# Kernel tuning notes

Measured on AMD Instinct MI355X. Metric: run time of the kernel, lower is better.

## Reference

```python
import jax, jax.numpy as jnp
import numpy as np

EPS = 1e-5


def _segment_norm(x, seg, num_segments):
    # x: [N, D], seg: [N] sorted segment ids in [0, num_segments)
    ones = jnp.ones((x.shape[0],), x.dtype)
    cnt = jax.ops.segment_sum(ones, seg, num_segments=num_segments)      # [B]
    safe = jnp.maximum(cnt, 1.0)[:, None]                                # avoid 0-div
    mean = jax.ops.segment_sum(x, seg, num_segments=num_segments) / safe # [B, D]
    centered = x - mean[seg]
    var = jax.ops.segment_sum(centered * centered, seg, num_segments=num_segments) / safe
    std = jnp.sqrt(var)                                                  # unbiased=False
    normed = centered / (std[seg] + EPS)
    # graphs with a single element are passed through unchanged
    return jnp.where((cnt > 1.0)[seg][:, None], normed, x)


def setup_inputs() -> dict:
    key = jax.random.key(0)
    k1, k2, k3, k4 = jax.random.split(key, 4)
    N, D, B = 1_000_000, 128, 1024
    node_feat = jax.random.normal(k1, (N, D), dtype=jnp.float32)
    edge_feat = jax.random.normal(k2, (N, D), dtype=jnp.float32)
    node_seg = jnp.sort(jax.random.randint(k3, (N,), 0, B, dtype=jnp.int32))
    edge_seg = jnp.sort(jax.random.randint(k4, (N,), 0, B, dtype=jnp.int32))
    return {
        "node_feat": node_feat,
        "edge_feat": edge_feat,
        "node_gamma": jnp.ones((D,), jnp.float32),
        "node_beta": jnp.zeros((D,), jnp.float32),
        "edge_gamma": jnp.ones((D,), jnp.float32),
        "edge_beta": jnp.zeros((D,), jnp.float32),
        "node_seg": node_seg,
        "edge_seg": edge_seg,
        "num_graphs": B,
    }


def reference(node_feat, edge_feat, node_gamma, node_beta, edge_gamma, edge_beta,
              node_seg, edge_seg, num_graphs):
    node_out = _segment_norm(node_feat, node_seg, num_graphs) * node_gamma + node_beta
    edge_out = _segment_norm(edge_feat, edge_seg, num_graphs) * edge_gamma + edge_beta
    return (node_out, edge_out)
```

## Files before the change

### kernel.cpp

```cpp
#include <hip/hip_runtime.h>


static constexpr int   D4     = 32;
static constexpr int   CHUNK  = 64;
static constexpr int   NCHUNK = 4;
static constexpr int   TILE_W = CHUNK * NCHUNK;
static constexpr int   TILE_B = TILE_W * 4;
static constexpr int   DEPTH  = 3;
static constexpr float EPS    = 1e-5f;

typedef float vfloat4 __attribute__((ext_vector_type(4)));

#define WAITV(N) do { asm volatile("s_waitcnt vmcnt(" #N ")" ::: "memory"); \
                      __builtin_amdgcn_sched_barrier(0); } while (0)

__device__ __forceinline__ void waitv_dyn(int n) {
    switch (n) {
        case 0:  WAITV(0);  break;
        case 4:  WAITV(4);  break;
        case 8:  WAITV(8);  break;
        case 12: WAITV(12); break;
        default: WAITV(16); break;
    }
}

__device__ __forceinline__ void nt_store4(float4* p, const float4& v) {
    vfloat4 w = { v.x, v.y, v.z, v.w };
    __builtin_nontemporal_store(w, reinterpret_cast<vfloat4*>(p));
}

__device__ __forceinline__ void acc4(float4& s, float4& q, const float4& v) {
    s.x += v.x; s.y += v.y; s.z += v.z; s.w += v.w;
    q.x += v.x * v.x; q.y += v.y * v.y;
    q.z += v.z * v.z; q.w += v.w * v.w;
}

__device__ __forceinline__ float4 affine4(const float4& v, const float4& A,
                                          const float4& Bc) {
    float4 o;
    o.x = v.x * A.x + Bc.x; o.y = v.y * A.y + Bc.y;
    o.z = v.z * A.z + Bc.z; o.w = v.w * A.w + Bc.w;
    return o;
}

__global__ __launch_bounds__(256) void seg_norm_r11(
    const float4* __restrict__ xn, const float4* __restrict__ xe,
    const float*  __restrict__ gn, const float*  __restrict__ bn,
    const float*  __restrict__ ge, const float*  __restrict__ be,
    const int*    __restrict__ sn, const int*    __restrict__ se,
    float4* __restrict__ on, float4* __restrict__ oe,
    int N)
{
    __shared__ float4 ring[4][DEPTH][TILE_W];
    __shared__ float4 pS[4][32], pQ[4][32];
    __shared__ int    s_bounds[2];

    const bool is_edge = (blockIdx.y != 0);
    const float4* __restrict__ x   = is_edge ? xe : xn;
    const float*  __restrict__ gam = is_edge ? ge : gn;
    const float*  __restrict__ bet = is_edge ? be : bn;
    const int*    __restrict__ seg = is_edge ? se : sn;
    float4*       __restrict__ out = is_edge ? oe : on;

    const int b   = (int)blockIdx.x;
    const int tid = (int)threadIdx.x;

    if (tid < 2) {
        const int target = b + tid;
        int lo = 0, hi = N;
        while (lo < hi) {
            int mid = (lo + hi) >> 1;
            if (seg[mid] < target) lo = mid + 1; else hi = mid;
        }
        s_bounds[tid] = lo;
    }
    __syncthreads();
    const int start = s_bounds[0];
    const int end   = s_bounds[1];
    const int cnt   = end - start;
    if (cnt <= 0) return;

    const int w    = tid >> 6;
    const int lane = tid & 63;
    const int dg   = lane & 31;

    const size_t f4base = (size_t)start * D4;
    const int    f4cnt  = cnt * D4;
    const int    nt     = f4cnt / TILE_B;

    auto issue = [&](int t, float4* lp) {
        const float4* gp = x + f4base + (size_t)t * TILE_B + w * TILE_W + lane;
        #pragma unroll
        for (int i = 0; i < NCHUNK; ++i)
            __builtin_amdgcn_global_load_lds(gp + i * CHUNK, lp + i * CHUNK, 16, 0, 0);
    };

    float4 s = make_float4(0.f, 0.f, 0.f, 0.f);
    float4 q = make_float4(0.f, 0.f, 0.f, 0.f);
    if (nt > 0) {
        const int pre = min(nt, DEPTH);
        for (int p = 0; p < pre; ++p) issue(p, &ring[w][p][0]);
        for (int t = 0; t < nt; ++t) {
            waitv_dyn(4 * min(DEPTH - 1, nt - 1 - t));
            float4* cur = &ring[w][t % DEPTH][0];
            #pragma unroll
            for (int i = 0; i < NCHUNK; ++i)
                acc4(s, q, cur[i * CHUNK + lane]);
            if (t + DEPTH < nt) issue(t + DEPTH, cur);
        }
    }
    for (int j = nt * TILE_B + tid; j < f4cnt; j += 256)
        acc4(s, q, x[f4base + j]);

    s.x += __shfl_down(s.x, 32); s.y += __shfl_down(s.y, 32);
    s.z += __shfl_down(s.z, 32); s.w += __shfl_down(s.w, 32);
    q.x += __shfl_down(q.x, 32); q.y += __shfl_down(q.y, 32);
    q.z += __shfl_down(q.z, 32); q.w += __shfl_down(q.w, 32);
    if (lane < 32) { pS[w][lane] = s; pQ[w][lane] = q; }
    __syncthreads();
    if (tid < 32) {
        float4 S = pS[0][tid], Q = pQ[0][tid];
        #pragma unroll
        for (int k = 1; k < 4; ++k) {
            const float4 a = pS[k][tid], c = pQ[k][tid];
            S.x += a.x; S.y += a.y; S.z += a.z; S.w += a.w;
            Q.x += c.x; Q.y += c.y; Q.z += c.z; Q.w += c.w;
        }
        const float rc = 1.0f / (float)cnt;
        float4 m, iv;
        m.x = S.x * rc; m.y = S.y * rc; m.z = S.z * rc; m.w = S.w * rc;
        iv.x = 1.0f / (sqrtf(fmaxf(Q.x * rc - m.x * m.x, 0.f)) + EPS);
        iv.y = 1.0f / (sqrtf(fmaxf(Q.y * rc - m.y * m.y, 0.f)) + EPS);
        iv.z = 1.0f / (sqrtf(fmaxf(Q.z * rc - m.z * m.z, 0.f)) + EPS);
        iv.w = 1.0f / (sqrtf(fmaxf(Q.w * rc - m.w * m.w, 0.f)) + EPS);
        if (cnt <= 1) {
            m  = make_float4(0.f, 0.f, 0.f, 0.f);
            iv = make_float4(1.f, 1.f, 1.f, 1.f);
        }
        const float4 g4 = ((const float4*)gam)[tid];
        const float4 b4 = ((const float4*)bet)[tid];
        float4 A, Bc;
        A.x = iv.x * g4.x; A.y = iv.y * g4.y; A.z = iv.z * g4.z; A.w = iv.w * g4.w;
        Bc.x = b4.x - m.x * A.x; Bc.y = b4.y - m.y * A.y;
        Bc.z = b4.z - m.z * A.z; Bc.w = b4.w - m.w * A.w;
        pS[0][tid] = A; pQ[0][tid] = Bc;
    }
    __syncthreads();
    const float4 A  = pS[0][dg];
    const float4 Bc = pQ[0][dg];

    if (nt > 0) {
        const int pre = min(nt, DEPTH);
        for (int p = 0; p < pre; ++p) issue(p, &ring[w][p][0]);
        for (int t = 0; t < nt; ++t) {
            waitv_dyn(4 * min(DEPTH - 1, nt - 1 - t) + 4 * min(DEPTH - 1, t));
            float4* cur = &ring[w][t % DEPTH][0];
            float4* op  = out + f4base + (size_t)t * TILE_B + w * TILE_W + lane;
            #pragma unroll
            for (int i = 0; i < NCHUNK; ++i)
                nt_store4(op + i * CHUNK, affine4(cur[i * CHUNK + lane], A, Bc));
            if (t + DEPTH < nt) issue(t + DEPTH, cur);
        }
    }
    for (int j = nt * TILE_B + tid; j < f4cnt; j += 256)
        nt_store4(&out[f4base + j], affine4(x[f4base + j], A, Bc));
}

extern "C" void kernel_launch(void* const* d_in, const int* in_sizes, int n_in,
                              void* d_out, int out_size, void* d_ws, size_t ws_size,
                              hipStream_t stream) {
    const float* node_feat  = (const float*)d_in[0];
    const float* edge_feat  = (const float*)d_in[1];
    const float* node_gamma = (const float*)d_in[2];
    const float* node_beta  = (const float*)d_in[3];
    const float* edge_gamma = (const float*)d_in[4];
    const float* edge_beta  = (const float*)d_in[5];
    const int*   node_seg   = (const int*)d_in[6];
    const int*   edge_seg   = (const int*)d_in[7];

    const int D = in_sizes[2];
    const int N = in_sizes[0] / D;
    const int B = 1024;

    float* out_node = (float*)d_out;
    float* out_edge = out_node + (size_t)N * (size_t)D;

    dim3 grid((unsigned)B, 2);
    seg_norm_r11<<<grid, 256, 0, stream>>>(
        (const float4*)node_feat, (const float4*)edge_feat,
        node_gamma, node_beta, edge_gamma, edge_beta,
        node_seg, edge_seg,
        (float4*)out_node, (float4*)out_edge, N);
}
```

Baseline: 566.5 us.

## Defer node-segment writeback to partner blocks via workspace flags and lagged scheduling

```diff
diff --git a/kernel.cpp b/kernel.cpp
--- a/kernel.cpp
+++ b/kernel.cpp
@@ -6,7 +6,7 @@
 static constexpr int   NCHUNK = 4;
 static constexpr int   TILE_W = CHUNK * NCHUNK;
 static constexpr int   TILE_B = TILE_W * 4;
-static constexpr int   DEPTH  = 3;
+static constexpr int   DEPTH  = 4;
 static constexpr float EPS    = 1e-5f;
 
 typedef float vfloat4 __attribute__((ext_vector_type(4)));
@@ -19,8 +19,7 @@
         case 0:  WAITV(0);  break;
         case 4:  WAITV(4);  break;
         case 8:  WAITV(8);  break;
-        case 12: WAITV(12); break;
-        default: WAITV(16); break;
+        default: WAITV(12); break;
     }
 }
 
@@ -43,47 +42,124 @@
     return o;
 }
 
-__global__ __launch_bounds__(256) void seg_norm_r11(
+__global__ __launch_bounds__(256) void seg_norm_lag(
     const float4* __restrict__ xn, const float4* __restrict__ xe,
     const float*  __restrict__ gn, const float*  __restrict__ bn,
     const float*  __restrict__ ge, const float*  __restrict__ be,
     const int*    __restrict__ sn, const int*    __restrict__ se,
     float4* __restrict__ on, float4* __restrict__ oe,
-    int N)
+    int* __restrict__ wsF, float4* __restrict__ wsA, float4* __restrict__ wsB,
+    int N, int lagmode)
 {
     __shared__ float4 ring[4][DEPTH][TILE_W];
     __shared__ float4 pS[4][32], pQ[4][32];
-    __shared__ int    s_bounds[2];
-
-    const bool is_edge = (blockIdx.y != 0);
-    const float4* __restrict__ x   = is_edge ? xe : xn;
-    const float*  __restrict__ gam = is_edge ? ge : gn;
-    const float*  __restrict__ bet = is_edge ? be : bn;
-    const int*    __restrict__ seg = is_edge ? se : sn;
-    float4*       __restrict__ out = is_edge ? oe : on;
-
-    const int b   = (int)blockIdx.x;
-    const int tid = (int)threadIdx.x;
-
-    if (tid < 2) {
-        const int target = b + tid;
-        int lo = 0, hi = N;
-        while (lo < hi) {
-            int mid = (lo + hi) >> 1;
-            if (seg[mid] < target) lo = mid + 1; else hi = mid;
-        }
-        s_bounds[tid] = lo;
-    }
-    __syncthreads();
-    const int start = s_bounds[0];
-    const int end   = s_bounds[1];
+    __shared__ float4 sAb[32], sBb[32];
+    __shared__ int    sm[4];
+
+    const int  bid  = (int)blockIdx.x;
+    const int  tid  = (int)threadIdx.x;
+    const int  w    = tid >> 6;
+    const int  lane = tid & 63;
+    const int  dg   = tid & 31;
+    const bool is_edge = (bid & 1);
+    const bool even    = !is_edge;
+
+    const float4* __restrict__ x    = is_edge ? xe : xn;
+    float4*       __restrict__ outp = is_edge ? oe : on;
+    const float*  __restrict__ gam  = is_edge ? ge : gn;
+    const float*  __restrict__ bet  = is_edge ? be : bn;
+    const int*    __restrict__ segp = is_edge ? se : sn;
+
+    auto bsearch2 = [&](const int* sg, int seg_id) {
+        if (tid < 2) {
+            const int target = seg_id + tid;
+            int lo = 0, hi = N;
+            while (lo < hi) {
+                int mid = (lo + hi) >> 1;
+                if (sg[mid] < target) lo = mid + 1; else hi = mid;
+            }
+            sm[tid] = lo;
+        }
+        __syncthreads();
+    };
+
+    auto fold_broadcast = [&](float4 s, float4 q, int cnt) {
+        s.x += __shfl_down(s.x, 32); s.y += __shfl_down(s.y, 32);
+        s.z += __shfl_down(s.z, 32); s.w += __shfl_down(s.w, 32);
+        q.x += __shfl_down(q.x, 32); q.y += __shfl_down(q.y, 32);
+        q.z += __shfl_down(q.z, 32); q.w += __shfl_down(q.w, 32);
+        if (lane < 32) { pS[w][lane] = s; pQ[w][lane] = q; }
+        __syncthreads();
+        if (tid < 32) {
+            float4 S = pS[0][tid], Q = pQ[0][tid];
+            #pragma unroll
+            for (int k = 1; k < 4; ++k) {
+                const float4 a = pS[k][tid], c = pQ[k][tid];
+                S.x += a.x; S.y += a.y; S.z += a.z; S.w += a.w;
+                Q.x += c.x; Q.y += c.y; Q.z += c.z; Q.w += c.w;
+            }
+            const float rc = 1.0f / (float)max(cnt, 1);
+            float4 m, iv;
+            m.x = S.x * rc; m.y = S.y * rc; m.z = S.z * rc; m.w = S.w * rc;
+            iv.x = 1.0f / (sqrtf(fmaxf(Q.x * rc - m.x * m.x, 0.f)) + EPS);
+            iv.y = 1.0f / (sqrtf(fmaxf(Q.y * rc - m.y * m.y, 0.f)) + EPS);
+            iv.z = 1.0f / (sqrtf(fmaxf(Q.z * rc - m.z * m.z, 0.f)) + EPS);
+            iv.w = 1.0f / (sqrtf(fmaxf(Q.w * rc - m.w * m.w, 0.f)) + EPS);
+            if (cnt <= 1) {
+                m  = make_float4(0.f, 0.f, 0.f, 0.f);
+                iv = make_float4(1.f, 1.f, 1.f, 1.f);
+            }
+            const float4 g4 = ((const float4*)gam)[tid];
+            const float4 b4 = ((const float4*)bet)[tid];
+            float4 A, Bc;
+            A.x = iv.x * g4.x; A.y = iv.y * g4.y;
+            A.z = iv.z * g4.z; A.w = iv.w * g4.w;
+            Bc.x = b4.x - m.x * A.x; Bc.y = b4.y - m.y * A.y;
+            Bc.z = b4.z - m.z * A.z; Bc.w = b4.w - m.w * A.w;
+            sAb[tid] = A; sBb[tid] = Bc;
+        }
+        __syncthreads();
+    };
+
+    auto bwrite = [&](const float4* src, float4* dst, size_t fb, int fc,
+                      float4 A, float4 Bc) {
+        int j = tid;
+        for (; j + 768 < fc; j += 1024) {
+            const float4 v0 = src[fb + j];
+            const float4 v1 = src[fb + j + 256];
+            const float4 v2 = src[fb + j + 512];
+            const float4 v3 = src[fb + j + 768];
+            nt_store4(&dst[fb + j],       affine4(v0, A, Bc));
+            nt_store4(&dst[fb + j + 256], affine4(v1, A, Bc));
+            nt_store4(&dst[fb + j + 512], affine4(v2, A, Bc));
+            nt_store4(&dst[fb + j + 768], affine4(v3, A, Bc));
+        }
+        for (; j < fc; j += 256)
+            nt_store4(&dst[fb + j], affine4(src[fb + j], A, Bc));
+    };
+
+    const bool has_partner = lagmode && even && (bid >= 512);
+    const int  pslot = (bid - 512) >> 1;
+    bool pre = false;
+    if (has_partner) {
+        if (tid == 0)
+            sm[2] = __hip_atomic_load(&wsF[pslot], __ATOMIC_ACQUIRE,
+                                      __HIP_MEMORY_SCOPE_AGENT);
+        __syncthreads();
+        pre = (sm[2] != 0);
+        if (pre) {
+            bsearch2(sn, pslot);
+            const int pst = sm[0], pen = sm[1];
+            const float4 A  = wsA[(size_t)pslot * 32 + dg];
+            const float4 Bc = wsB[(size_t)pslot * 32 + dg];
+            bwrite(xn, on, (size_t)pst * D4, (pen - pst) * D4, A, Bc);
+        }
+        __syncthreads();
+    }
+
+    bsearch2(segp, bid >> 1);
+    const int start = sm[0], end = sm[1];
     const int cnt   = end - start;
-    if (cnt <= 0) return;
-
-    const int w    = tid >> 6;
-    const int lane = tid & 63;
-    const int dg   = lane & 31;
-
     const size_t f4base = (size_t)start * D4;
     const int    f4cnt  = cnt * D4;
     const int    nt     = f4cnt / TILE_B;
@@ -98,11 +174,11 @@
     float4 s = make_float4(0.f, 0.f, 0.f, 0.f);
     float4 q = make_float4(0.f, 0.f, 0.f, 0.f);
     if (nt > 0) {
-        const int pre = min(nt, DEPTH);
-        for (int p = 0; p < pre; ++p) issue(p, &ring[w][p][0]);
+        const int preN = min(nt, DEPTH);
+        for (int p = 0; p < preN; ++p) issue(p, &ring[w][p][0]);
         for (int t = 0; t < nt; ++t) {
             waitv_dyn(4 * min(DEPTH - 1, nt - 1 - t));
-            float4* cur = &ring[w][t % DEPTH][0];
+            float4* cur = &ring[w][t & (DEPTH - 1)][0];
             #pragma unroll
             for (int i = 0; i < NCHUNK; ++i)
                 acc4(s, q, cur[i * CHUNK + lane]);
@@ -112,58 +188,60 @@
     for (int j = nt * TILE_B + tid; j < f4cnt; j += 256)
         acc4(s, q, x[f4base + j]);
 
-    s.x += __shfl_down(s.x, 32); s.y += __shfl_down(s.y, 32);
-    s.z += __shfl_down(s.z, 32); s.w += __shfl_down(s.w, 32);
-    q.x += __shfl_down(q.x, 32); q.y += __shfl_down(q.y, 32);
-    q.z += __shfl_down(q.z, 32); q.w += __shfl_down(q.w, 32);
-    if (lane < 32) { pS[w][lane] = s; pQ[w][lane] = q; }
-    __syncthreads();
-    if (tid < 32) {
-        float4 S = pS[0][tid], Q = pQ[0][tid];
-        #pragma unroll
-        for (int k = 1; k < 4; ++k) {
-            const float4 a = pS[k][tid], c = pQ[k][tid];
-            S.x += a.x; S.y += a.y; S.z += a.z; S.w += a.w;
-            Q.x += c.x; Q.y += c.y; Q.z += c.z; Q.w += c.w;
-        }
-        const float rc = 1.0f / (float)cnt;
-        float4 m, iv;
-        m.x = S.x * rc; m.y = S.y * rc; m.z = S.z * rc; m.w = S.w * rc;
-        iv.x = 1.0f / (sqrtf(fmaxf(Q.x * rc - m.x * m.x, 0.f)) + EPS);
-        iv.y = 1.0f / (sqrtf(fmaxf(Q.y * rc - m.y * m.y, 0.f)) + EPS);
-        iv.z = 1.0f / (sqrtf(fmaxf(Q.z * rc - m.z * m.z, 0.f)) + EPS);
-        iv.w = 1.0f / (sqrtf(fmaxf(Q.w * rc - m.w * m.w, 0.f)) + EPS);
-        if (cnt <= 1) {
-            m  = make_float4(0.f, 0.f, 0.f, 0.f);
-            iv = make_float4(1.f, 1.f, 1.f, 1.f);
-        }
-        const float4 g4 = ((const float4*)gam)[tid];
-        const float4 b4 = ((const float4*)bet)[tid];
+    fold_broadcast(s, q, cnt);
+
+    if (lagmode && even) {
+        const int slot = bid >> 1;
+        if (tid < 32) {
+            wsA[(size_t)slot * 32 + tid] = sAb[tid];
+            wsB[(size_t)slot * 32 + tid] = sBb[tid];
+        }
+        __threadfence();
+        if (tid == 0)
+            __hip_atomic_store(&wsF[slot], 1, __ATOMIC_RELEASE,
+                               __HIP_MEMORY_SCOPE_AGENT);
+    }
+
+    if (!lagmode || !even) {
+        bwrite(x, outp, f4base, f4cnt, sAb[dg], sBb[dg]);
+        return;
+    }
+
+    if (bid >= 1536)
+        bwrite(x, outp, f4base, f4cnt, sAb[dg], sBb[dg]);
+
+    if (has_partner && !pre) {
+        if (tid == 0) {
+            int got = 0;
+            for (int it = 0; it < 1200 && !got; ++it) {
+                got = __hip_atomic_load(&wsF[pslot], __ATOMIC_ACQUIRE,
+                                        __HIP_MEMORY_SCOPE_AGENT);
+                if (!got) __builtin_amdgcn_s_sleep(16);
+            }
+            sm[2] = got;
+        }
+        __syncthreads();
+        const bool got = (sm[2] != 0);
+        __syncthreads();
+        bsearch2(sn, pslot);
+        const int pst = sm[0], pen = sm[1];
+        const int pcnt = pen - pst;
+        const size_t pfb = (size_t)pst * D4;
+        const int    pfc = pcnt * D4;
         float4 A, Bc;
-        A.x = iv.x * g4.x; A.y = iv.y * g4.y; A.z = iv.z * g4.z; A.w = iv.w * g4.w;
-        Bc.x = b4.x - m.x * A.x; Bc.y = b4.y - m.y * A.y;
-        Bc.z = b4.z - m.z * A.z; Bc.w = b4.w - m.w * A.w;
-        pS[0][tid] = A; pQ[0][tid] = Bc;
-    }
-    __syncthreads();
-    const float4 A  = pS[0][dg];
-    const float4 Bc = pQ[0][dg];
-
-    if (nt > 0) {
-        const int pre = min(nt, DEPTH);
-        for (int p = 0; p < pre; ++p) issue(p, &ring[w][p][0]);
-        for (int t = 0; t < nt; ++t) {
-            waitv_dyn(4 * min(DEPTH - 1, nt - 1 - t) + 4 * min(DEPTH - 1, t));
-            float4* cur = &ring[w][t % DEPTH][0];
-            float4* op  = out + f4base + (size_t)t * TILE_B + w * TILE_W + lane;
-            #pragma unroll
-            for (int i = 0; i < NCHUNK; ++i)
-                nt_store4(op + i * CHUNK, affine4(cur[i * CHUNK + lane], A, Bc));
-            if (t + DEPTH < nt) issue(t + DEPTH, cur);
-        }
-    }
-    for (int j = nt * TILE_B + tid; j < f4cnt; j += 256)
-        nt_store4(&out[f4base + j], affine4(x[f4base + j], A, Bc));
+        if (got) {
+            A  = wsA[(size_t)pslot * 32 + dg];
+            Bc = wsB[(size_t)pslot * 32 + dg];
+        } else {
+            float4 fs = make_float4(0.f, 0.f, 0.f, 0.f);
+            float4 fq = make_float4(0.f, 0.f, 0.f, 0.f);
+            for (int j = tid; j < pfc; j += 256)
+                acc4(fs, fq, xn[pfb + j]);
+            fold_broadcast(fs, fq, pcnt);
+            A = sAb[dg]; Bc = sBb[dg];
+        }
+        bwrite(xn, on, pfb, pfc, A, Bc);
+    }
 }
 
 extern "C" void kernel_launch(void* const* d_in, const int* in_sizes, int n_in,
@@ -185,10 +263,18 @@
     float* out_node = (float*)d_out;
     float* out_edge = out_node + (size_t)N * (size_t)D;
 
-    dim3 grid((unsigned)B, 2);
-    seg_norm_r11<<<grid, 256, 0, stream>>>(
+    const size_t need = 4096 + 2ull * 1024 * 32 * sizeof(float4);
+    int lagmode = (ws_size >= need) ? 1 : 0;
+    int*    wsF = (int*)d_ws;
+    float4* wsA = (float4*)((char*)d_ws + 4096);
+    float4* wsB = wsA + 1024 * 32;
+    if (lagmode)
+        hipMemsetAsync(d_ws, 0, 4096, stream);
+
+    seg_norm_lag<<<dim3(2u * B), 256, 0, stream>>>(
         (const float4*)node_feat, (const float4*)edge_feat,
         node_gamma, node_beta, edge_gamma, edge_beta,
         node_seg, edge_seg,
-        (float4*)out_node, (float4*)out_edge, N);
-}
+        (float4*)out_node, (float4*)out_edge,
+        wsF, wsA, wsB, N, lagmode);
+}
```

New measurement: 965.7 us. 1.7x slower.

## Split segments across blocks, cache tile in registers, combine stats via atomics

Applied to the files above, without the earlier changes.

```diff
diff --git a/kernel.cpp b/kernel.cpp
--- a/kernel.cpp
+++ b/kernel.cpp
@@ -1,28 +1,12 @@
 #include <hip/hip_runtime.h>
 
 
-static constexpr int   D4     = 32;
-static constexpr int   CHUNK  = 64;
-static constexpr int   NCHUNK = 4;
-static constexpr int   TILE_W = CHUNK * NCHUNK;
-static constexpr int   TILE_B = TILE_W * 4;
-static constexpr int   DEPTH  = 3;
-static constexpr float EPS    = 1e-5f;
+static constexpr int   RV       = 32;
+static constexpr int   CHUNK_F4 = RV * 256;
+static constexpr int   CPS      = 5;
+static constexpr float EPS      = 1e-5f;
 
 typedef float vfloat4 __attribute__((ext_vector_type(4)));
-
-#define WAITV(N) do { asm volatile("s_waitcnt vmcnt(" #N ")" ::: "memory"); \
-                      __builtin_amdgcn_sched_barrier(0); } while (0)
-
-__device__ __forceinline__ void waitv_dyn(int n) {
-    switch (n) {
-        case 0:  WAITV(0);  break;
-        case 4:  WAITV(4);  break;
-        case 8:  WAITV(8);  break;
-        case 12: WAITV(12); break;
-        default: WAITV(16); break;
-    }
-}
 
 __device__ __forceinline__ void nt_store4(float4* p, const float4& v) {
     vfloat4 w = { v.x, v.y, v.z, v.w };
@@ -43,74 +27,71 @@
     return o;
 }
 
-__global__ __launch_bounds__(256) void seg_norm_r11(
+__global__ __launch_bounds__(256) void seg_norm_reg(
     const float4* __restrict__ xn, const float4* __restrict__ xe,
     const float*  __restrict__ gn, const float*  __restrict__ bn,
     const float*  __restrict__ ge, const float*  __restrict__ be,
     const int*    __restrict__ sn, const int*    __restrict__ se,
     float4* __restrict__ on, float4* __restrict__ oe,
-    int N)
+    int* __restrict__ wsCnt, int* __restrict__ wsFlag,
+    float4* __restrict__ wsA, float4* __restrict__ wsB,
+    float4* __restrict__ wsP, int N)
 {
-    __shared__ float4 ring[4][DEPTH][TILE_W];
     __shared__ float4 pS[4][32], pQ[4][32];
-    __shared__ int    s_bounds[2];
-
+    __shared__ float4 sA[32], sB[32];
+    __shared__ int    sm[4];
+
+    const int  bx     = (int)blockIdx.x;
+    const int  segid  = bx / CPS;
+    const int  c      = bx % CPS;
     const bool is_edge = (blockIdx.y != 0);
-    const float4* __restrict__ x   = is_edge ? xe : xn;
-    const float*  __restrict__ gam = is_edge ? ge : gn;
-    const float*  __restrict__ bet = is_edge ? be : bn;
-    const int*    __restrict__ seg = is_edge ? se : sn;
-    float4*       __restrict__ out = is_edge ? oe : on;
-
-    const int b   = (int)blockIdx.x;
-    const int tid = (int)threadIdx.x;
+    const int  slot   = (is_edge ? 1024 : 0) + segid;
+    const int  tid    = (int)threadIdx.x;
+    const int  w      = tid >> 6;
+    const int  lane   = tid & 63;
+    const int  dg     = tid & 31;
+
+    const float4* __restrict__ x    = is_edge ? xe : xn;
+    float4*       __restrict__ outp = is_edge ? oe : on;
+    const float*  __restrict__ gam  = is_edge ? ge : gn;
+    const float*  __restrict__ bet  = is_edge ? be : bn;
+    const int*    __restrict__ seg  = is_edge ? se : sn;
 
     if (tid < 2) {
-        const int target = b + tid;
+        const int target = segid + tid;
         int lo = 0, hi = N;
         while (lo < hi) {
             int mid = (lo + hi) >> 1;
             if (seg[mid] < target) lo = mid + 1; else hi = mid;
         }
-        s_bounds[tid] = lo;
-    }
-    __syncthreads();
-    const int start = s_bounds[0];
-    const int end   = s_bounds[1];
+        sm[tid] = lo;
+    }
+    __syncthreads();
+    const int start = sm[0], end = sm[1];
     const int cnt   = end - start;
     if (cnt <= 0) return;
 
-    const int w    = tid >> 6;
-    const int lane = tid & 63;
-    const int dg   = lane & 31;
-
-    const size_t f4base = (size_t)start * D4;
-    const int    f4cnt  = cnt * D4;
-    const int    nt     = f4cnt / TILE_B;
-
-    auto issue = [&](int t, float4* lp) {
-        const float4* gp = x + f4base + (size_t)t * TILE_B + w * TILE_W + lane;
-        #pragma unroll
-        for (int i = 0; i < NCHUNK; ++i)
-            __builtin_amdgcn_global_load_lds(gp + i * CHUNK, lp + i * CHUNK, 16, 0, 0);
-    };
-
+    const int f4cnt = cnt * 32;
+    const int nb    = min((f4cnt + CHUNK_F4 - 1) / CHUNK_F4, CPS);
+    if (c >= nb) return;
+    const size_t fb   = (size_t)start * 32;
+    const int    coff = c * CHUNK_F4;
+    const int    rem  = f4cnt - coff;
+
+    const float4* src_ = x + fb + coff;
+    float4 cache[RV];
+    #pragma unroll
+    for (int k = 0; k < RV; ++k) {
+        const int idx = k * 256 + tid;
+        cache[k] = (idx < rem) ? src_[idx] : make_float4(0.f, 0.f, 0.f, 0.f);
+    }
     float4 s = make_float4(0.f, 0.f, 0.f, 0.f);
     float4 q = make_float4(0.f, 0.f, 0.f, 0.f);
-    if (nt > 0) {
-        const int pre = min(nt, DEPTH);
-        for (int p = 0; p < pre; ++p) issue(p, &ring[w][p][0]);
-        for (int t = 0; t < nt; ++t) {
-            waitv_dyn(4 * min(DEPTH - 1, nt - 1 - t));
-            float4* cur = &ring[w][t % DEPTH][0];
-            #pragma unroll
-            for (int i = 0; i < NCHUNK; ++i)
-                acc4(s, q, cur[i * CHUNK + lane]);
-            if (t + DEPTH < nt) issue(t + DEPTH, cur);
-        }
-    }
-    for (int j = nt * TILE_B + tid; j < f4cnt; j += 256)
-        acc4(s, q, x[f4base + j]);
+    #pragma unroll
+    for (int k = 0; k < RV; ++k) acc4(s, q, cache[k]);
+    if (c == CPS - 1)
+        for (int j = CPS * CHUNK_F4 + tid; j < f4cnt; j += 256)
+            acc4(s, q, x[fb + j]);
 
     s.x += __shfl_down(s.x, 32); s.y += __shfl_down(s.y, 32);
     s.z += __shfl_down(s.z, 32); s.w += __shfl_down(s.w, 32);
@@ -118,13 +99,134 @@
     q.z += __shfl_down(q.z, 32); q.w += __shfl_down(q.w, 32);
     if (lane < 32) { pS[w][lane] = s; pQ[w][lane] = q; }
     __syncthreads();
+
+    const size_t pbase = ((size_t)slot * CPS + c) * 64;
     if (tid < 32) {
         float4 S = pS[0][tid], Q = pQ[0][tid];
         #pragma unroll
         for (int k = 1; k < 4; ++k) {
-            const float4 a = pS[k][tid], c = pQ[k][tid];
+            const float4 a = pS[k][tid], cc = pQ[k][tid];
             S.x += a.x; S.y += a.y; S.z += a.z; S.w += a.w;
-            Q.x += c.x; Q.y += c.y; Q.z += c.z; Q.w += c.w;
+            Q.x += cc.x; Q.y += cc.y; Q.z += cc.z; Q.w += cc.w;
+        }
+        wsP[pbase + tid]      = S;
+        wsP[pbase + 32 + tid] = Q;
+    }
+    __syncthreads();
+    if (tid == 0) {
+        __threadfence();
+        const int prev = __hip_atomic_fetch_add(&wsCnt[slot], 1,
+                             __ATOMIC_ACQ_REL, __HIP_MEMORY_SCOPE_AGENT);
+        sm[2] = (prev == nb - 1);
+    }
+    __syncthreads();
+
+    if (sm[2]) {
+        if (tid < 32) {
+            float4 S = make_float4(0.f, 0.f, 0.f, 0.f);
+            float4 Q = make_float4(0.f, 0.f, 0.f, 0.f);
+            for (int cc = 0; cc < nb; ++cc) {
+                const size_t pb = ((size_t)slot * CPS + cc) * 64;
+                const float4 a = wsP[pb + tid], b2 = wsP[pb + 32 + tid];
+                S.x += a.x; S.y += a.y; S.z += a.z; S.w += a.w;
+                Q.x += b2.x; Q.y += b2.y; Q.z += b2.z; Q.w += b2.w;
+            }
+            const float rc = 1.0f / (float)cnt;
+            float4 m, iv;
+            m.x = S.x * rc; m.y = S.y * rc; m.z = S.z * rc; m.w = S.w * rc;
+            iv.x = 1.0f / (sqrtf(fmaxf(Q.x * rc - m.x * m.x, 0.f)) + EPS);
+            iv.y = 1.0f / (sqrtf(fmaxf(Q.y * rc - m.y * m.y, 0.f)) + EPS);
+            iv.z = 1.0f / (sqrtf(fmaxf(Q.z * rc - m.z * m.z, 0.f)) + EPS);
+            iv.w = 1.0f / (sqrtf(fmaxf(Q.w * rc - m.w * m.w, 0.f)) + EPS);
+            if (cnt <= 1) {
+                m  = make_float4(0.f, 0.f, 0.f, 0.f);
+                iv = make_float4(1.f, 1.f, 1.f, 1.f);
+            }
+            const float4 g4 = ((const float4*)gam)[tid];
+            const float4 b4 = ((const float4*)bet)[tid];
+            float4 A, Bc;
+            A.x = iv.x * g4.x; A.y = iv.y * g4.y;
+            A.z = iv.z * g4.z; A.w = iv.w * g4.w;
+            Bc.x = b4.x - m.x * A.x; Bc.y = b4.y - m.y * A.y;
+            Bc.z = b4.z - m.z * A.z; Bc.w = b4.w - m.w * A.w;
+            wsA[(size_t)slot * 32 + tid] = A;
+            wsB[(size_t)slot * 32 + tid] = Bc;
+        }
+        __syncthreads();
+        if (tid == 0) {
+            __threadfence();
+            __hip_atomic_store(&wsFlag[slot], 1,
+                               __ATOMIC_RELEASE, __HIP_MEMORY_SCOPE_AGENT);
+        }
+    }
+
+    if (tid == 0) {
+        while (!__hip_atomic_load(&wsFlag[slot], __ATOMIC_ACQUIRE,
+                                  __HIP_MEMORY_SCOPE_AGENT))
+            __builtin_amdgcn_s_sleep(8);
+    }
+    __syncthreads();
+    if (tid < 32) {
+        sA[tid] = wsA[(size_t)slot * 32 + tid];
+        sB[tid] = wsB[(size_t)slot * 32 + tid];
+    }
+    __syncthreads();
+    const float4 A  = sA[dg];
+    const float4 Bc = sB[dg];
+
+    float4* dst_ = outp + fb + coff;
+    #pragma unroll
+    for (int k = 0; k < RV; ++k) {
+        const int idx = k * 256 + tid;
+        if (idx < rem) nt_store4(&dst_[idx], affine4(cache[k], A, Bc));
+    }
+    if (c == CPS - 1)
+        for (int j = CPS * CHUNK_F4 + tid; j < f4cnt; j += 256)
+            nt_store4(&outp[fb + j], affine4(x[fb + j], A, Bc));
+}
+
+__global__ __launch_bounds__(256) void seg_norm_simple(
+    const float4* __restrict__ xn, const float4* __restrict__ xe,
+    const float*  __restrict__ gn, const float*  __restrict__ bn,
+    const float*  __restrict__ ge, const float*  __restrict__ be,
+    const int*    __restrict__ sn, const int*    __restrict__ se,
+    float4* __restrict__ on, float4* __restrict__ oe, int N)
+{
+    __shared__ float4 pS[4][32], pQ[4][32];
+    __shared__ int sm[2];
+    const bool is_edge = (blockIdx.y != 0);
+    const float4* x = is_edge ? xe : xn;
+    const float* gam = is_edge ? ge : gn;
+    const float* bet = is_edge ? be : bn;
+    const int* seg = is_edge ? se : sn;
+    float4* out = is_edge ? oe : on;
+    const int b = (int)blockIdx.x, tid = (int)threadIdx.x;
+    const int w = tid >> 6, lane = tid & 63, dg = tid & 31;
+    if (tid < 2) {
+        const int target = b + tid; int lo = 0, hi = N;
+        while (lo < hi) { int mid = (lo + hi) >> 1;
+            if (seg[mid] < target) lo = mid + 1; else hi = mid; }
+        sm[tid] = lo;
+    }
+    __syncthreads();
+    const int start = sm[0], end = sm[1], cnt = end - start;
+    if (cnt <= 0) return;
+    const size_t fb = (size_t)start * 32; const int fc = cnt * 32;
+    float4 s = make_float4(0,0,0,0), q = make_float4(0,0,0,0);
+    for (int j = tid; j < fc; j += 256) acc4(s, q, x[fb + j]);
+    s.x += __shfl_down(s.x, 32); s.y += __shfl_down(s.y, 32);
+    s.z += __shfl_down(s.z, 32); s.w += __shfl_down(s.w, 32);
+    q.x += __shfl_down(q.x, 32); q.y += __shfl_down(q.y, 32);
+    q.z += __shfl_down(q.z, 32); q.w += __shfl_down(q.w, 32);
+    if (lane < 32) { pS[w][lane] = s; pQ[w][lane] = q; }
+    __syncthreads();
+    if (tid < 32) {
+        float4 S = pS[0][tid], Q = pQ[0][tid];
+        #pragma unroll
+        for (int k = 1; k < 4; ++k) {
+            const float4 a = pS[k][tid], c2 = pQ[k][tid];
+            S.x += a.x; S.y += a.y; S.z += a.z; S.w += a.w;
+            Q.x += c2.x; Q.y += c2.y; Q.z += c2.z; Q.w += c2.w;
         }
         const float rc = 1.0f / (float)cnt;
         float4 m, iv;
@@ -133,37 +235,19 @@
         iv.y = 1.0f / (sqrtf(fmaxf(Q.y * rc - m.y * m.y, 0.f)) + EPS);
         iv.z = 1.0f / (sqrtf(fmaxf(Q.z * rc - m.z * m.z, 0.f)) + EPS);
         iv.w = 1.0f / (sqrtf(fmaxf(Q.w * rc - m.w * m.w, 0.f)) + EPS);
-        if (cnt <= 1) {
-            m  = make_float4(0.f, 0.f, 0.f, 0.f);
-            iv = make_float4(1.f, 1.f, 1.f, 1.f);
-        }
+        if (cnt <= 1) { m = make_float4(0,0,0,0); iv = make_float4(1,1,1,1); }
         const float4 g4 = ((const float4*)gam)[tid];
         const float4 b4 = ((const float4*)bet)[tid];
         float4 A, Bc;
-        A.x = iv.x * g4.x; A.y = iv.y * g4.y; A.z = iv.z * g4.z; A.w = iv.w * g4.w;
-        Bc.x = b4.x - m.x * A.x; Bc.y = b4.y - m.y * A.y;
-        Bc.z = b4.z - m.z * A.z; Bc.w = b4.w - m.w * A.w;
+        A.x = iv.x*g4.x; A.y = iv.y*g4.y; A.z = iv.z*g4.z; A.w = iv.w*g4.w;
+        Bc.x = b4.x - m.x*A.x; Bc.y = b4.y - m.y*A.y;
+        Bc.z = b4.z - m.z*A.z; Bc.w = b4.w - m.w*A.w;
         pS[0][tid] = A; pQ[0][tid] = Bc;
     }
     __syncthreads();
-    const float4 A  = pS[0][dg];
-    const float4 Bc = pQ[0][dg];
-
-    if (nt > 0) {
-        const int pre = min(nt, DEPTH);
-        for (int p = 0; p < pre; ++p) issue(p, &ring[w][p][0]);
-        for (int t = 0; t < nt; ++t) {
-            waitv_dyn(4 * min(DEPTH - 1, nt - 1 - t) + 4 * min(DEPTH - 1, t));
-            float4* cur = &ring[w][t % DEPTH][0];
-            float4* op  = out + f4base + (size_t)t * TILE_B + w * TILE_W + lane;
-            #pragma unroll
-            for (int i = 0; i < NCHUNK; ++i)
-                nt_store4(op + i * CHUNK, affine4(cur[i * CHUNK + lane], A, Bc));
-            if (t + DEPTH < nt) issue(t + DEPTH, cur);
-        }
-    }
-    for (int j = nt * TILE_B + tid; j < f4cnt; j += 256)
-        nt_store4(&out[f4base + j], affine4(x[f4base + j], A, Bc));
+    const float4 A = pS[0][dg], Bc = pQ[0][dg];
+    for (int j = tid; j < fc; j += 256)
+        nt_store4(&out[fb + j], affine4(x[fb + j], A, Bc));
 }
 
 extern "C" void kernel_launch(void* const* d_in, const int* in_sizes, int n_in,
@@ -185,10 +269,27 @@
     float* out_node = (float*)d_out;
     float* out_edge = out_node + (size_t)N * (size_t)D;
 
-    dim3 grid((unsigned)B, 2);
-    seg_norm_r11<<<grid, 256, 0, stream>>>(
-        (const float4*)node_feat, (const float4*)edge_feat,
-        node_gamma, node_beta, edge_gamma, edge_beta,
-        node_seg, edge_seg,
-        (float4*)out_node, (float4*)out_edge, N);
-}
+    const size_t offFlag = 2048 * sizeof(int);
+    const size_t offA    = 16384;
+    const size_t offB    = offA + (size_t)2048 * 32 * 16;
+    const size_t offP    = offB + (size_t)2048 * 32 * 16;
+    const size_t need    = offP + (size_t)2048 * CPS * 64 * 16;
+
+    if (ws_size >= need) {
+        hipMemsetAsync(d_ws, 0, offA, stream);
+        seg_norm_reg<<<dim3((unsigned)(B * CPS), 2), 256, 0, stream>>>(
+            (const float4*)node_feat, (const float4*)edge_feat,
+            node_gamma, node_beta, edge_gamma, edge_beta,
+            node_seg, edge_seg,
+            (float4*)out_node, (float4*)out_edge,
+            (int*)d_ws, (int*)((char*)d_ws + offFlag),
+            (float4*)((char*)d_ws + offA), (float4*)((char*)d_ws + offB),
+            (float4*)((char*)d_ws + offP), N);
+    } else {
+        seg_norm_simple<<<dim3((unsigned)B, 2), 256, 0, stream>>>(
+            (const float4*)node_feat, (const float4*)edge_feat,
+            node_gamma, node_beta, edge_gamma, edge_beta,
+            node_seg, edge_seg,
+            (float4*)out_node, (float4*)out_edge, N);
+    }
+}
```

After: 1.884 ms. 3.33x slower.

## Cache segment rows in registers to avoid re-reading input for normalization pass

Applied to the files above, without the earlier changes.

```diff
diff --git a/kernel.cpp b/kernel.cpp
--- a/kernel.cpp
+++ b/kernel.cpp
@@ -1,28 +1,11 @@
 #include <hip/hip_runtime.h>
 
 
-static constexpr int   D4     = 32;
-static constexpr int   CHUNK  = 64;
-static constexpr int   NCHUNK = 4;
-static constexpr int   TILE_W = CHUNK * NCHUNK;
-static constexpr int   TILE_B = TILE_W * 4;
-static constexpr int   DEPTH  = 3;
-static constexpr float EPS    = 1e-5f;
+static constexpr int   RV  = 88;
+static constexpr int   CAP = RV * 256;
+static constexpr float EPS = 1e-5f;
 
 typedef float vfloat4 __attribute__((ext_vector_type(4)));
-
-#define WAITV(N) do { asm volatile("s_waitcnt vmcnt(" #N ")" ::: "memory"); \
-                      __builtin_amdgcn_sched_barrier(0); } while (0)
-
-__device__ __forceinline__ void waitv_dyn(int n) {
-    switch (n) {
-        case 0:  WAITV(0);  break;
-        case 4:  WAITV(4);  break;
-        case 8:  WAITV(8);  break;
-        case 12: WAITV(12); break;
-        default: WAITV(16); break;
-    }
-}
 
 __device__ __forceinline__ void nt_store4(float4* p, const float4& v) {
     vfloat4 w = { v.x, v.y, v.z, v.w };
@@ -43,7 +26,7 @@
     return o;
 }
 
-__global__ __launch_bounds__(256) void seg_norm_r11(
+__global__ __launch_bounds__(256, 1) void seg_norm_rr(
     const float4* __restrict__ xn, const float4* __restrict__ xe,
     const float*  __restrict__ gn, const float*  __restrict__ bn,
     const float*  __restrict__ ge, const float*  __restrict__ be,
@@ -51,119 +34,136 @@
     float4* __restrict__ on, float4* __restrict__ oe,
     int N)
 {
-    __shared__ float4 ring[4][DEPTH][TILE_W];
     __shared__ float4 pS[4][32], pQ[4][32];
-    __shared__ int    s_bounds[2];
+    __shared__ int    sm[4];
 
-    const bool is_edge = (blockIdx.y != 0);
-    const float4* __restrict__ x   = is_edge ? xe : xn;
-    const float*  __restrict__ gam = is_edge ? ge : gn;
-    const float*  __restrict__ bet = is_edge ? be : bn;
-    const int*    __restrict__ seg = is_edge ? se : sn;
-    float4*       __restrict__ out = is_edge ? oe : on;
+    const int b    = (int)blockIdx.x;
+    const int tid  = (int)threadIdx.x;
+    const int w    = tid >> 6;
+    const int lane = tid & 63;
+    const int dg   = tid & 31;
 
-    const int b   = (int)blockIdx.x;
-    const int tid = (int)threadIdx.x;
-
-    if (tid < 2) {
-        const int target = b + tid;
+    if (tid < 4) {
+        const int* sg    = (tid < 2) ? sn : se;
+        const int target = b + (tid & 1);
         int lo = 0, hi = N;
         while (lo < hi) {
             int mid = (lo + hi) >> 1;
-            if (seg[mid] < target) lo = mid + 1; else hi = mid;
+            if (sg[mid] < target) lo = mid + 1; else hi = mid;
         }
-        s_bounds[tid] = lo;
+        sm[tid] = lo;
     }
     __syncthreads();
-    const int start = s_bounds[0];
-    const int end   = s_bounds[1];
-    const int cnt   = end - start;
-    if (cnt <= 0) return;
+    const int st0 = sm[0], cnt0 = sm[1] - sm[0];
+    const int st1 = sm[2], cnt1 = sm[3] - sm[2];
+    const size_t fb0 = (size_t)st0 * 32;  const int fc0 = cnt0 * 32;
+    const size_t fb1 = (size_t)st1 * 32;  const int fc1 = cnt1 * 32;
 
-    const int w    = tid >> 6;
-    const int lane = tid & 63;
-    const int dg   = lane & 31;
-
-    const size_t f4base = (size_t)start * D4;
-    const int    f4cnt  = cnt * D4;
-    const int    nt     = f4cnt / TILE_B;
-
-    auto issue = [&](int t, float4* lp) {
-        const float4* gp = x + f4base + (size_t)t * TILE_B + w * TILE_W + lane;
-        #pragma unroll
-        for (int i = 0; i < NCHUNK; ++i)
-            __builtin_amdgcn_global_load_lds(gp + i * CHUNK, lp + i * CHUNK, 16, 0, 0);
+    auto fold = [&](float4 s, float4 q, int cnt,
+                    const float* gam, const float* bet,
+                    float4& A_out, float4& Bc_out) {
+        s.x += __shfl_down(s.x, 32); s.y += __shfl_down(s.y, 32);
+        s.z += __shfl_down(s.z, 32); s.w += __shfl_down(s.w, 32);
+        q.x += __shfl_down(q.x, 32); q.y += __shfl_down(q.y, 32);
+        q.z += __shfl_down(q.z, 32); q.w += __shfl_down(q.w, 32);
+        __syncthreads();
+        if (lane < 32) { pS[w][lane] = s; pQ[w][lane] = q; }
+        __syncthreads();
+        if (tid < 32) {
+            float4 S = pS[0][tid], Q = pQ[0][tid];
+            #pragma unroll
+            for (int k = 1; k < 4; ++k) {
+                const float4 a = pS[k][tid], c = pQ[k][tid];
+                S.x += a.x; S.y += a.y; S.z += a.z; S.w += a.w;
+                Q.x += c.x; Q.y += c.y; Q.z += c.z; Q.w += c.w;
+            }
+            const float rc = 1.0f / (float)max(cnt, 1);
+            float4 m, iv;
+            m.x = S.x * rc; m.y = S.y * rc; m.z = S.z * rc; m.w = S.w * rc;
+            iv.x = 1.0f / (sqrtf(fmaxf(Q.x * rc - m.x * m.x, 0.f)) + EPS);
+            iv.y = 1.0f / (sqrtf(fmaxf(Q.y * rc - m.y * m.y, 0.f)) + EPS);
+            iv.z = 1.0f / (sqrtf(fmaxf(Q.z * rc - m.z * m.z, 0.f)) + EPS);
+            iv.w = 1.0f / (sqrtf(fmaxf(Q.w * rc - m.w * m.w, 0.f)) + EPS);
+            if (cnt <= 1) {
+                m  = make_float4(0.f, 0.f, 0.f, 0.f);
+                iv = make_float4(1.f, 1.f, 1.f, 1.f);
+            }
+            const float4 g4 = ((const float4*)gam)[tid];
+            const float4 b4 = ((const float4*)bet)[tid];
+            float4 A, Bc;
+            A.x = iv.x * g4.x; A.y = iv.y * g4.y;
+            A.z = iv.z * g4.z; A.w = iv.w * g4.w;
+            Bc.x = b4.x - m.x * A.x; Bc.y = b4.y - m.y * A.y;
+            Bc.z = b4.z - m.z * A.z; Bc.w = b4.w - m.w * A.w;
+            pS[0][tid] = A; pQ[0][tid] = Bc;
+        }
+        __syncthreads();
+        A_out = pS[0][dg]; Bc_out = pQ[0][dg];
     };
 
-    float4 s = make_float4(0.f, 0.f, 0.f, 0.f);
-    float4 q = make_float4(0.f, 0.f, 0.f, 0.f);
-    if (nt > 0) {
-        const int pre = min(nt, DEPTH);
-        for (int p = 0; p < pre; ++p) issue(p, &ring[w][p][0]);
-        for (int t = 0; t < nt; ++t) {
-            waitv_dyn(4 * min(DEPTH - 1, nt - 1 - t));
-            float4* cur = &ring[w][t % DEPTH][0];
+    float4 cache[RV];
+    float4 s, q, A0, Bc0, A1, Bc1;
+
+    s = make_float4(0.f, 0.f, 0.f, 0.f);
+    q = make_float4(0.f, 0.f, 0.f, 0.f);
+    if (cnt0 > 0) {
+        const int hi0 = fc0 - 1;
+        #pragma unroll
+        for (int k = 0; k < RV; ++k) {
+            const int idx = k * 256 + tid;
+            cache[k] = xn[fb0 + (size_t)min(idx, hi0)];
+        }
+        #pragma unroll
+        for (int k = 0; k < RV; ++k) {
+            const int idx = k * 256 + tid;
+            float4 v = cache[k];
+            if (idx >= fc0) v = make_float4(0.f, 0.f, 0.f, 0.f);
+            acc4(s, q, v);
+        }
+        for (int j = CAP + tid; j < fc0; j += 256)
+            acc4(s, q, xn[fb0 + j]);
+    }
+    fold(s, q, cnt0, gn, bn, A0, Bc0);
+
+    s = make_float4(0.f, 0.f, 0.f, 0.f);
+    q = make_float4(0.f, 0.f, 0.f, 0.f);
+    {
+        const int hi1 = (cnt1 > 0) ? (fc1 - 1) : 0;
+        #pragma unroll
+        for (int k = 0; k < RV; ++k) {
+            const int idx = k * 256 + tid;
+            if (cnt0 > 0 && idx < fc0)
+                nt_store4(&on[fb0 + idx], affine4(cache[k], A0, Bc0));
+            if (cnt1 > 0)
+                cache[k] = xe[fb1 + (size_t)min(idx, hi1)];
+        }
+        if (cnt0 > 0)
+            for (int j = CAP + tid; j < fc0; j += 256)
+                nt_store4(&on[fb0 + j], affine4(xn[fb0 + j], A0, Bc0));
+        if (cnt1 > 0) {
             #pragma unroll
-            for (int i = 0; i < NCHUNK; ++i)
-                acc4(s, q, cur[i * CHUNK + lane]);
-            if (t + DEPTH < nt) issue(t + DEPTH, cur);
+            for (int k = 0; k < RV; ++k) {
+                const int idx = k * 256 + tid;
+                float4 v = cache[k];
+                if (idx >= fc1) v = make_float4(0.f, 0.f, 0.f, 0.f);
+                acc4(s, q, v);
+            }
+            for (int j = CAP + tid; j < fc1; j += 256)
+                acc4(s, q, xe[fb1 + j]);
         }
     }
-    for (int j = nt * TILE_B + tid; j < f4cnt; j += 256)
-        acc4(s, q, x[f4base + j]);
+    fold(s, q, cnt1, ge, be, A1, Bc1);
 
-    s.x += __shfl_down(s.x, 32); s.y += __shfl_down(s.y, 32);
-    s.z += __shfl_down(s.z, 32); s.w += __shfl_down(s.w, 32);
-    q.x += __shfl_down(q.x, 32); q.y += __shfl_down(q.y, 32);
-    q.z += __shfl_down(q.z, 32); q.w += __shfl_down(q.w, 32);
-    if (lane < 32) { pS[w][lane] = s; pQ[w][lane] = q; }
-    __syncthreads();
-    if (tid < 32) {
-        float4 S = pS[0][tid], Q = pQ[0][tid];
+    if (cnt1 > 0) {
         #pragma unroll
-        for (int k = 1; k < 4; ++k) {
-            const float4 a = pS[k][tid], c = pQ[k][tid];
-            S.x += a.x; S.y += a.y; S.z += a.z; S.w += a.w;
-            Q.x += c.x; Q.y += c.y; Q.z += c.z; Q.w += c.w;
+        for (int k = 0; k < RV; ++k) {
+            const int idx = k * 256 + tid;
+            if (idx < fc1)
+                nt_store4(&oe[fb1 + idx], affine4(cache[k], A1, Bc1));
         }
-        const float rc = 1.0f / (float)cnt;
-        float4 m, iv;
-        m.x = S.x * rc; m.y = S.y * rc; m.z = S.z * rc; m.w = S.w * rc;
-        iv.x = 1.0f / (sqrtf(fmaxf(Q.x * rc - m.x * m.x, 0.f)) + EPS);
-        iv.y = 1.0f / (sqrtf(fmaxf(Q.y * rc - m.y * m.y, 0.f)) + EPS);
-        iv.z = 1.0f / (sqrtf(fmaxf(Q.z * rc - m.z * m.z, 0.f)) + EPS);
-        iv.w = 1.0f / (sqrtf(fmaxf(Q.w * rc - m.w * m.w, 0.f)) + EPS);
-        if (cnt <= 1) {
-            m  = make_float4(0.f, 0.f, 0.f, 0.f);
-            iv = make_float4(1.f, 1.f, 1.f, 1.f);
-        }
-        const float4 g4 = ((const float4*)gam)[tid];
-        const float4 b4 = ((const float4*)bet)[tid];
-        float4 A, Bc;
-        A.x = iv.x * g4.x; A.y = iv.y * g4.y; A.z = iv.z * g4.z; A.w = iv.w * g4.w;
-        Bc.x = b4.x - m.x * A.x; Bc.y = b4.y - m.y * A.y;
-        Bc.z = b4.z - m.z * A.z; Bc.w = b4.w - m.w * A.w;
-        pS[0][tid] = A; pQ[0][tid] = Bc;
+        for (int j = CAP + tid; j < fc1; j += 256)
+            nt_store4(&oe[fb1 + j], affine4(xe[fb1 + j], A1, Bc1));
     }
-    __syncthreads();
-    const float4 A  = pS[0][dg];
-    const float4 Bc = pQ[0][dg];
-
-    if (nt > 0) {
-        const int pre = min(nt, DEPTH);
-        for (int p = 0; p < pre; ++p) issue(p, &ring[w][p][0]);
-        for (int t = 0; t < nt; ++t) {
-            waitv_dyn(4 * min(DEPTH - 1, nt - 1 - t) + 4 * min(DEPTH - 1, t));
-            float4* cur = &ring[w][t % DEPTH][0];
-            float4* op  = out + f4base + (size_t)t * TILE_B + w * TILE_W + lane;
-            #pragma unroll
-            for (int i = 0; i < NCHUNK; ++i)
-                nt_store4(op + i * CHUNK, affine4(cur[i * CHUNK + lane], A, Bc));
-            if (t + DEPTH < nt) issue(t + DEPTH, cur);
-        }
-    }
-    for (int j = nt * TILE_B + tid; j < f4cnt; j += 256)
-        nt_store4(&out[f4base + j], affine4(x[f4base + j], A, Bc));
 }
 
 extern "C" void kernel_launch(void* const* d_in, const int* in_sizes, int n_in,
@@ -185,8 +185,7 @@
     float* out_node = (float*)d_out;
     float* out_edge = out_node + (size_t)N * (size_t)D;
 
-    dim3 grid((unsigned)B, 2);
-    seg_norm_r11<<<grid, 256, 0, stream>>>(
+    seg_norm_rr<<<dim3((unsigned)B), 256, 0, stream>>>(
         (const float4*)node_feat, (const float4*)edge_feat,
         node_gamma, node_beta, edge_gamma, edge_beta,
         node_seg, edge_seg,
```

Result: slower. 686.3 us (+21.1%).
